# Kernel optimization log

Measured on AMD Instinct MI355X. Metric: run time of the kernel, lower is better.

The kernel has to match this reference:

```python
import jax, jax.numpy as jnp
import numpy as np

D_STATE = 8
D_CONV = 4
DT_RANK = 8
THRESHOLD = 0.5
KPOOL = 3
PAD = (KPOOL - 1) // 2
EPS = 1e-5


def _rmsnorm(x, w):
    return x * jax.lax.rsqrt(jnp.mean(x * x, axis=-1, keepdims=True) + EPS) * w


def _dw_causal_conv(x, w, b):
    # x: (L, T, C), w: (C, 1, K) depthwise causal conv along T
    xt = jnp.transpose(x, (0, 2, 1))  # (L, C, T)
    y = jax.lax.conv_general_dilated(
        xt, w, window_strides=(1,), padding=[(D_CONV - 1, 0)],
        dimension_numbers=('NCH', 'OIH', 'NCH'), feature_group_count=xt.shape[1])
    return jnp.transpose(y, (0, 2, 1)) + b


def _selective_scan(x, delta, A, B, Cm, D):
    # x, delta: (L,T,d); A: (d,n); B, Cm: (L,T,n); D: (d,)
    dA = jnp.exp(delta[..., None] * A)                        # (L,T,d,n)
    dBx = (delta * x)[..., None] * B[:, :, None, :]           # (L,T,d,n)
    def combine(a, b):
        a1, b1 = a
        a2, b2 = b
        return (a2 * a1, a2 * b1 + b2)
    _, h = jax.lax.associative_scan(combine, (dA, dBx), axis=1)
    y = jnp.einsum('ltdn,ltn->ltd', h, Cm)
    return y + x * D


def _mamba_block(x, in_proj, conv_w, conv_b, x_proj_w, dt_proj_w, dt_proj_b,
                 A_log_f, A_log_b, D_f, D_b, out_proj_w, rms_w):
    # single-depth bidirectional (bimamba-v2 style) block, expand=1, residual + RMSNorm
    res = x
    xn = _rmsnorm(x, rms_w)
    xz = xn @ in_proj                       # (L,T,2C)
    xi, z = jnp.split(xz, 2, axis=-1)
    xi = jax.nn.silu(_dw_causal_conv(xi, conv_w, conv_b))
    dbl = xi @ x_proj_w                     # (L,T,dt_rank+2*d_state)
    dt = dbl[..., :DT_RANK]
    Bm = dbl[..., DT_RANK:DT_RANK + D_STATE]
    Cm = dbl[..., DT_RANK + D_STATE:]
    delta = jax.nn.softplus(dt @ dt_proj_w + dt_proj_b)
    A_f = -jnp.exp(A_log_f)
    A_b = -jnp.exp(A_log_b)
    flip = lambda a: a[:, ::-1]
    y_f = _selective_scan(xi, delta, A_f, Bm, Cm, D_f)
    y_b = flip(_selective_scan(flip(xi), flip(delta), A_b, flip(Bm), flip(Cm), D_b))
    y = 0.5 * (y_f + y_b) * jax.nn.silu(z)  # if_devide_out -> average two directions
    return res + y @ out_proj_w


def reference(feats, in_proj, conv_w, conv_b, x_proj_w, dt_proj_w, dt_proj_b,
              A_log_f, A_log_b, D_f, D_b, out_proj_w, rms_w, mlp_w, mlp_b,
              record_len):
    N, C, H, W = feats.shape
    T = H * W
    rec = np.asarray(record_len)  # static ragged group sizes
    ends = np.cumsum(rec)
    starts = ends - rec
    masks = []
    for s0, L in zip(starts.tolist(), rec.tolist()):
        g = feats[s0:s0 + L]                       # (L,C,H,W)
        if L > 1:
            x = g.reshape(L, C, T).transpose(0, 2, 1)  # l c h w -> l (h w) c
            feat = _mamba_block(x, in_proj, conv_w, conv_b, x_proj_w, dt_proj_w,
                                dt_proj_b, A_log_f, A_log_b, D_f, D_b,
                                out_proj_w, rms_w)
            score = jax.nn.sigmoid(feat @ mlp_w + mlp_b)   # (L,T,1)
            ego = jnp.ones((1, T, 1), feats.dtype)
            bs = jnp.concatenate([ego, score[1:]], axis=0)
        else:
            bs = jnp.ones((1, T, 1), feats.dtype)
        bs = bs.transpose(0, 2, 1).reshape(L, 1, H, W)     # l (h w) c -> l c h w
        masks.append(jnp.where(bs > THRESHOLD, 1.0, 0.0).astype(feats.dtype))
    mask = jnp.concatenate(masks, axis=0)                  # (N,1,H,W)
    pooled = jax.lax.reduce_window(
        mask, -jnp.inf, jax.lax.max,
        window_dimensions=(1, 1, KPOOL, KPOOL), window_strides=(1, 1, 1, 1),
        padding=[(0, 0), (0, 0), (PAD, PAD), (PAD, PAD)])
    return pooled


def setup_inputs():
    key = jax.random.key(0)
    ks = jax.random.split(key, 8)
    C, H, W = 128, 96, 96
    record_len = np.array([2, 3, 1, 2, 4], dtype=np.int64)
    N = int(record_len.sum())
    s = 0.05
    A_log = jnp.log(jnp.broadcast_to(
        jnp.arange(1, D_STATE + 1, dtype=jnp.float32), (C, D_STATE)))
    return {
        'feats': jax.random.normal(ks[0], (N, C, H, W), jnp.float32),
        'in_proj': jax.random.normal(ks[1], (C, 2 * C), jnp.float32) * s,
        'conv_w': jax.random.normal(ks[2], (C, 1, D_CONV), jnp.float32) * s,
        'conv_b': jnp.zeros((C,), jnp.float32),
        'x_proj_w': jax.random.normal(ks[3], (C, DT_RANK + 2 * D_STATE), jnp.float32) * s,
        'dt_proj_w': jax.random.normal(ks[4], (DT_RANK, C), jnp.float32) * s,
        'dt_proj_b': jnp.full((C,), 0.1, jnp.float32),
        'A_log_f': A_log,
        'A_log_b': A_log,
        'D_f': jnp.ones((C,), jnp.float32),
        'D_b': jnp.ones((C,), jnp.float32),
        'out_proj_w': jax.random.normal(ks[5], (C, C), jnp.float32) * s,
        'rms_w': jnp.ones((C,), jnp.float32),
        'mlp_w': jax.random.normal(ks[6], (C, 1), jnp.float32) * s,
        'mlp_b': jnp.zeros((1,), jnp.float32),
        'record_len': jnp.asarray(record_len),
    }
```

## Files before the change

### kernel.cpp

```cpp
#include <hip/hip_runtime.h>
#include <cstdint>
#include <cstddef>

#define C_CH 128
#define T_TOK 9216
#define H_IMG 96
#define W_IMG 96
#define NSTATE 8

#define CHUNK 128
#define RHALO 32
#define REGION (CHUNK + 2 * RHALO)

__device__ __forceinline__ float siluf_dev(float x) {
  return x / (1.0f + expf(-x));
}

__device__ __forceinline__ float fast_silu(float x) {
  return __fdividef(x, 1.0f + __expf(-x));
}

__global__ __launch_bounds__(128) void k0_setup(
    const int* __restrict__ rec, int n_groups, int N,
    const float* __restrict__ out_proj_w, const float* __restrict__ mlp_w,
    float* __restrict__ vvec, int* __restrict__ slot)
{
  const int tid = threadIdx.x;
  if (tid == 0) {
    int f = 0, sl = 0;
    for (int g = 0; g < n_groups; ++g) {
      const int L = rec[g];
      slot[f] = -1;
      for (int i = 1; i < L; ++i) slot[f + i] = sl++;
      f += L;
    }
  }
  if (tid < C_CH) {
    float acc = 0.0f;
    for (int j = 0; j < C_CH; ++j) acc += out_proj_w[tid * C_CH + j] * mlp_w[j];
    vvec[tid] = acc;
  }
}

__global__ __launch_bounds__(256) void k1_gemm(
    const float* __restrict__ feats, const float* __restrict__ in_proj,
    const float* __restrict__ rms_w, const float* __restrict__ mlp_w,
    const float* __restrict__ mlp_b, const float* __restrict__ vvec,
    const int* __restrict__ slot,
    float* __restrict__ xipre, float* __restrict__ wbuf,
    float* __restrict__ logit)
{
  __shared__ float Asm[C_CH * 64];
  __shared__ float Bsm[C_CH * 64];
  __shared__ float redA[256], redB[256], irS[64];
  const int f = blockIdx.y;
  const int s = slot[f];
  if (s < 0) return;
  const int m0 = blockIdx.x * 64;
  const int tid = threadIdx.x;

  {
    const int c0 = tid >> 4;
    const int tq = (tid & 15) * 4;
    const float* src = feats + (size_t)f * C_CH * T_TOK + m0 + tq;
    #pragma unroll
    for (int i = 0; i < 8; ++i) {
      const int c = c0 + i * 16;
      const float4 x4 = *(const float4*)(src + (size_t)c * T_TOK);
      *(float4*)&Asm[c * 64 + tq] = x4;
    }
  }
  __syncthreads();
  {
    const int t = tid & 63;
    const int q = tid >> 6;
    float ssum = 0.0f, rm = 0.0f;
    for (int cc = q * 32; cc < q * 32 + 32; ++cc) {
      const float val = Asm[cc * 64 + t];
      ssum += val * val;
      rm += val * mlp_w[cc];
    }
    redA[tid] = ssum; redB[tid] = rm;
  }
  __syncthreads();
  if (tid < 64) {
    const int t = tid;
    const float ssum = redA[t] + redA[t + 64] + redA[t + 128] + redA[t + 192];
    const float rm   = redB[t] + redB[t + 64] + redB[t + 128] + redB[t + 192];
    const float ir = 1.0f / sqrtf(ssum * (1.0f / C_CH) + 1e-5f);
    logit[(size_t)s * T_TOK + m0 + t] = rm + mlp_b[0];
    irS[t] = ir;
  }
  __syncthreads();
  {
    const int t = tid & 63;
    const int q = tid >> 6;
    const float ir = irS[t];
    for (int cc = q * 32; cc < q * 32 + 32; ++cc) Asm[cc * 64 + t] *= ir;
  }

  const int ti = tid >> 4;
  const int tc = tid & 15;
  for (int chunk = 0; chunk < 4; ++chunk) {
    const int n0 = chunk * 64;
    __syncthreads();
    #pragma unroll
    for (int i = 0; i < 8; ++i) {
      const int idx = tid + 256 * i;
      const int k = idx >> 4;
      const int q = (idx & 15) * 4;
      float4 b4 = *(const float4*)(in_proj + (size_t)k * 256 + n0 + q);
      const float rw = rms_w[k];
      b4.x *= rw; b4.y *= rw; b4.z *= rw; b4.w *= rw;
      *(float4*)&Bsm[k * 64 + q] = b4;
    }
    __syncthreads();
    float acc[4][4];
    #pragma unroll
    for (int i = 0; i < 4; ++i)
      #pragma unroll
      for (int j = 0; j < 4; ++j) acc[i][j] = 0.0f;
    #pragma unroll 8
    for (int k = 0; k < C_CH; ++k) {
      const float4 a4 = *(const float4*)&Asm[k * 64 + ti * 4];
      const float4 b4 = *(const float4*)&Bsm[k * 64 + tc * 4];
      acc[0][0] += a4.x * b4.x; acc[0][1] += a4.x * b4.y; acc[0][2] += a4.x * b4.z; acc[0][3] += a4.x * b4.w;
      acc[1][0] += a4.y * b4.x; acc[1][1] += a4.y * b4.y; acc[1][2] += a4.y * b4.z; acc[1][3] += a4.y * b4.w;
      acc[2][0] += a4.z * b4.x; acc[2][1] += a4.z * b4.y; acc[2][2] += a4.z * b4.z; acc[2][3] += a4.z * b4.w;
      acc[3][0] += a4.w * b4.x; acc[3][1] += a4.w * b4.y; acc[3][2] += a4.w * b4.z; acc[3][3] += a4.w * b4.w;
    }
    if (chunk < 2) {
      const int cb = n0 + tc * 4;
      #pragma unroll
      for (int i = 0; i < 4; ++i) {
        const int t = m0 + ti * 4 + i;
        float4 o; o.x = acc[i][0]; o.y = acc[i][1]; o.z = acc[i][2]; o.w = acc[i][3];
        *(float4*)&xipre[((size_t)s * T_TOK + t) * C_CH + cb] = o;
      }
    } else {
      const int zc = (chunk - 2) * 64 + tc * 4;
      const float4 v4 = *(const float4*)&vvec[zc];
      #pragma unroll
      for (int i = 0; i < 4; ++i) {
        const int t = m0 + ti * 4 + i;
        float4 o;
        o.x = 0.5f * siluf_dev(acc[i][0]) * v4.x;
        o.y = 0.5f * siluf_dev(acc[i][1]) * v4.y;
        o.z = 0.5f * siluf_dev(acc[i][2]) * v4.z;
        o.w = 0.5f * siluf_dev(acc[i][3]) * v4.w;
        *(float4*)&wbuf[((size_t)s * T_TOK + t) * C_CH + zc] = o;
      }
    }
  }
}

__global__ __launch_bounds__(256, 3) void k3_fused(
    const float* __restrict__ xipre, const float* __restrict__ wbuf,
    const float* __restrict__ conv_w, const float* __restrict__ conv_b,
    const float* __restrict__ x_proj_w,
    const float* __restrict__ dt_proj_w, const float* __restrict__ dt_proj_b,
    const float* __restrict__ A_log_f, const float* __restrict__ A_log_b,
    const float* __restrict__ D_f, const float* __restrict__ D_b,
    const int* __restrict__ slot, float* __restrict__ logit)
{
  __shared__ float xibuf[64 * 129];
  __shared__ float dbl[REGION * 24];
  const int f = blockIdx.y;
  const int s = slot[f];
  if (s < 0) return;
  const int c0 = blockIdx.x * CHUNK;
  const int r0 = c0 - RHALO;
  const int tid = threadIdx.x;
  const int c = tid & 127;
  const int half = tid >> 7;
  const size_t rowbase = (size_t)s * T_TOK;
  const float4 cw = *(const float4*)(conv_w + c * 4);
  const float cb = conv_b[c];

  auto ldx = [&](int t) -> float {
    return (t >= 0 && t < T_TOK) ? xipre[(rowbase + t) * C_CH + c] : 0.0f;
  };

  const int q6 = __builtin_amdgcn_readfirstlane(tid >> 6) * 6;
  const int tok = tid & 63;
  for (int pass = 0; pass < 3; ++pass) {
    __syncthreads();
    {
      const int prow0 = pass * 64 + half * 32;
      float xm1 = ldx(r0 + prow0 - 1);
      float xm2 = ldx(r0 + prow0 - 2);
      float xm3 = ldx(r0 + prow0 - 3);
      for (int i = 0; i < 32; ++i) {
        const float cur = ldx(r0 + prow0 + i);
        const float sum = cw.x * xm3 + cw.y * xm2 + cw.z * xm1 + cw.w * cur + cb;
        xibuf[(half * 32 + i) * 129 + c] = fast_silu(sum);
        xm3 = xm2; xm2 = xm1; xm1 = cur;
      }
    }
    __syncthreads();
    {
      float acc[6] = {0, 0, 0, 0, 0, 0};
      for (int cc = 0; cc < C_CH; ++cc) {
        const float xv = xibuf[tok * 129 + cc];
        #pragma unroll
        for (int jj = 0; jj < 6; ++jj)
          acc[jj] += xv * x_proj_w[cc * 24 + q6 + jj];
      }
      #pragma unroll
      for (int jj = 0; jj < 6; ++jj)
        dbl[(pass * 64 + tok) * 24 + q6 + jj] = acc[jj];
    }
  }
  __syncthreads();

  float dw[8], Ac[8];
  const float* Alog = half ? A_log_b : A_log_f;
  #pragma unroll
  for (int r = 0; r < 8; ++r) dw[r] = dt_proj_w[r * C_CH + c];
  #pragma unroll
  for (int n = 0; n < NSTATE; ++n) Ac[n] = -expf(Alog[c * NSTATE + n]);
  const float bias = dt_proj_b[c];
  const float Dd = half ? D_b[c] : D_f[c];
  float h[8] = {0, 0, 0, 0, 0, 0, 0, 0};

  const float a0 = Ac[0];
  int okl = 1;
  #pragma unroll
  for (int n = 1; n < NSTATE; ++n)
    okl &= (fabsf(Ac[n] - (float)(n + 1) * a0) <= 1e-4f * fabsf(Ac[n])) ? 1 : 0;
  const bool fastA = (__all(okl) != 0);

  auto decay8 = [&](float dlt, float* dA) {
    if (fastA) {
      const float e1 = __expf(dlt * a0);
      const float e2 = e1 * e1, e3 = e2 * e1, e4 = e2 * e2;
      dA[0] = e1; dA[1] = e2; dA[2] = e3; dA[3] = e4;
      dA[4] = e4 * e1; dA[5] = e4 * e2; dA[6] = e4 * e3; dA[7] = e4 * e4;
    } else {
      #pragma unroll
      for (int n = 0; n < NSTATE; ++n) dA[n] = __expf(dlt * Ac[n]);
    }
  };

  if (half == 0) {
    const int tb = (r0 < 0) ? 0 : r0;
    const int steps = c0 + CHUNK - tb;
    const int outg0 = (c0 - tb) >> 3;
    const int ng = steps >> 3;
    float xm1 = ldx(tb - 1), xm2 = ldx(tb - 2), xm3 = ldx(tb - 3);
    for (int g = 0; g < ng; ++g) {
      const int t0 = tb + g * 8;
      const bool out = (g >= outg0);
      float pg[8], wg[8];
      #pragma unroll
      for (int j = 0; j < 8; ++j) {
        const size_t gi = (rowbase + t0 + j) * C_CH + c;
        pg[j] = xipre[gi];
        wg[j] = out ? wbuf[gi] : 0.0f;
      }
      #pragma unroll
      for (int j = 0; j < 8; ++j) {
        const int t = t0 + j;
        const int p = t - r0;
        const float cur = pg[j];
        const float sum = cw.x * xm3 + cw.y * xm2 + cw.z * xm1 + cw.w * cur + cb;
        const float xiv = fast_silu(sum);
        xm3 = xm2; xm2 = xm1; xm1 = cur;
        const float4 d0 = *(const float4*)&dbl[p * 24];
        const float4 d1 = *(const float4*)&dbl[p * 24 + 4];
        float pre = bias;
        pre += d0.x * dw[0] + d0.y * dw[1] + d0.z * dw[2] + d0.w * dw[3];
        pre += d1.x * dw[4] + d1.y * dw[5] + d1.z * dw[6] + d1.w * dw[7];
        const float dlt = fmaxf(pre, 0.0f) + __logf(1.0f + __expf(-fabsf(pre)));
        const float u = dlt * xiv;
        const float4 b0 = *(const float4*)&dbl[p * 24 + 8];
        const float4 b1 = *(const float4*)&dbl[p * 24 + 12];
        float dA[8];
        decay8(dlt, dA);
        h[0] = dA[0] * h[0] + u * b0.x;
        h[1] = dA[1] * h[1] + u * b0.y;
        h[2] = dA[2] * h[2] + u * b0.z;
        h[3] = dA[3] * h[3] + u * b0.w;
        h[4] = dA[4] * h[4] + u * b1.x;
        h[5] = dA[5] * h[5] + u * b1.y;
        h[6] = dA[6] * h[6] + u * b1.z;
        h[7] = dA[7] * h[7] + u * b1.w;
        if (out) {
          const float4 cc0 = *(const float4*)&dbl[p * 24 + 16];
          const float4 cc1 = *(const float4*)&dbl[p * 24 + 20];
          float y = xiv * Dd;
          y += h[0] * cc0.x + h[1] * cc0.y + h[2] * cc0.z + h[3] * cc0.w;
          y += h[4] * cc1.x + h[5] * cc1.y + h[6] * cc1.z + h[7] * cc1.w;
          float contrib = y * wg[j];
          contrib += __shfl_xor(contrib, 1);
          contrib += __shfl_xor(contrib, 2);
          contrib += __shfl_xor(contrib, 4);
          contrib += __shfl_xor(contrib, 8);
          contrib += __shfl_xor(contrib, 16);
          contrib += __shfl_xor(contrib, 32);
          if ((tid & 63) == 0) atomicAdd(&logit[rowbase + t], contrib);
        }
      }
    }
  } else {
    const int te2e = r0 + REGION;
    const int te2 = (te2e > T_TOK) ? T_TOK : te2e;
    const int steps = te2 - c0;
    const int outg0 = (te2 - (c0 + CHUNK)) >> 3;
    const int ng = steps >> 3;
    float w0 = ldx(te2 - 1), w1 = ldx(te2 - 2), w2 = ldx(te2 - 3), w3 = ldx(te2 - 4);
    for (int g = 0; g < ng; ++g) {
      const int t0 = te2 - 1 - g * 8;
      const bool out = (g >= outg0);
      float nv[8], wg[8];
      #pragma unroll
      for (int j = 0; j < 8; ++j) {
        nv[j] = ldx(t0 - 4 - j);
        wg[j] = out ? wbuf[(rowbase + t0 - j) * C_CH + c] : 0.0f;
      }
      #pragma unroll
      for (int j = 0; j < 8; ++j) {
        const int t = t0 - j;
        const int p = t - r0;
        const float sum = cw.x * w3 + cw.y * w2 + cw.z * w1 + cw.w * w0 + cb;
        const float xiv = fast_silu(sum);
        w0 = w1; w1 = w2; w2 = w3; w3 = nv[j];
        const float4 d0 = *(const float4*)&dbl[p * 24];
        const float4 d1 = *(const float4*)&dbl[p * 24 + 4];
        float pre = bias;
        pre += d0.x * dw[0] + d0.y * dw[1] + d0.z * dw[2] + d0.w * dw[3];
        pre += d1.x * dw[4] + d1.y * dw[5] + d1.z * dw[6] + d1.w * dw[7];
        const float dlt = fmaxf(pre, 0.0f) + __logf(1.0f + __expf(-fabsf(pre)));
        const float u = dlt * xiv;
        const float4 b0 = *(const float4*)&dbl[p * 24 + 8];
        const float4 b1 = *(const float4*)&dbl[p * 24 + 12];
        float dA[8];
        decay8(dlt, dA);
        h[0] = dA[0] * h[0] + u * b0.x;
        h[1] = dA[1] * h[1] + u * b0.y;
        h[2] = dA[2] * h[2] + u * b0.z;
        h[3] = dA[3] * h[3] + u * b0.w;
        h[4] = dA[4] * h[4] + u * b1.x;
        h[5] = dA[5] * h[5] + u * b1.y;
        h[6] = dA[6] * h[6] + u * b1.z;
        h[7] = dA[7] * h[7] + u * b1.w;
        if (out) {
          const float4 cc0 = *(const float4*)&dbl[p * 24 + 16];
          const float4 cc1 = *(const float4*)&dbl[p * 24 + 20];
          float y = xiv * Dd;
          y += h[0] * cc0.x + h[1] * cc0.y + h[2] * cc0.z + h[3] * cc0.w;
          y += h[4] * cc1.x + h[5] * cc1.y + h[6] * cc1.z + h[7] * cc1.w;
          float contrib = y * wg[j];
          contrib += __shfl_xor(contrib, 1);
          contrib += __shfl_xor(contrib, 2);
          contrib += __shfl_xor(contrib, 4);
          contrib += __shfl_xor(contrib, 8);
          contrib += __shfl_xor(contrib, 16);
          contrib += __shfl_xor(contrib, 32);
          if ((tid & 63) == 0) atomicAdd(&logit[rowbase + t], contrib);
        }
      }
    }
  }
}

__global__ __launch_bounds__(128) void k4_pool(
    const float* __restrict__ logit, const int* __restrict__ slot,
    float* __restrict__ out)
{
  const int w = threadIdx.x;
  if (w >= W_IMG) return;
  const int hh = blockIdx.x;
  const int f = blockIdx.y;
  const int s = slot[f];
  float m = 0.0f;
  if (s < 0) {
    m = 1.0f;
  } else {
    for (int dh = -1; dh <= 1; ++dh) {
      const int h2 = hh + dh;
      if (h2 < 0 || h2 >= H_IMG) continue;
      for (int dw = -1; dw <= 1; ++dw) {
        const int w2 = w + dw;
        if (w2 < 0 || w2 >= W_IMG) continue;
        if (logit[(size_t)s * T_TOK + h2 * W_IMG + w2] > 0.0f) m = 1.0f;
      }
    }
  }
  out[(size_t)f * T_TOK + hh * W_IMG + w] = m;
}

extern "C" void kernel_launch(void* const* d_in, const int* in_sizes, int n_in,
                              void* d_out, int out_size, void* d_ws, size_t ws_size,
                              hipStream_t stream) {
  const float* feats      = (const float*)d_in[0];
  const float* in_proj    = (const float*)d_in[1];
  const float* conv_w     = (const float*)d_in[2];
  const float* conv_b     = (const float*)d_in[3];
  const float* x_proj_w   = (const float*)d_in[4];
  const float* dt_proj_w  = (const float*)d_in[5];
  const float* dt_proj_b  = (const float*)d_in[6];
  const float* A_log_f    = (const float*)d_in[7];
  const float* A_log_b    = (const float*)d_in[8];
  const float* D_f        = (const float*)d_in[9];
  const float* D_b        = (const float*)d_in[10];
  const float* out_proj_w = (const float*)d_in[11];
  const float* rms_w      = (const float*)d_in[12];
  const float* mlp_w      = (const float*)d_in[13];
  const float* mlp_b      = (const float*)d_in[14];
  const int*   rec        = (const int*)d_in[15];

  const int N = in_sizes[0] / (C_CH * T_TOK);
  const int n_groups = in_sizes[15];
  int S = N - n_groups;
  if (S < 1) S = 1;

  char* p = (char*)d_ws;
  float* vvec  = (float*)p; p += 1024;
  int*   slot  = (int*)p;   p += ((N * 4 + 255) / 256) * 256;
  float* logit = (float*)p; p += (size_t)S * T_TOK * 4;
  float* xipre = (float*)p; p += (size_t)S * T_TOK * C_CH * 4;
  float* wA    = (float*)p; p += (size_t)S * T_TOK * C_CH * 4;
  (void)ws_size; (void)n_in; (void)out_size;

  k0_setup<<<1, 128, 0, stream>>>(rec, n_groups, N, out_proj_w, mlp_w, vvec, slot);
  k1_gemm<<<dim3(T_TOK / 64, N), 256, 0, stream>>>(
      feats, in_proj, rms_w, mlp_w, mlp_b, vvec, slot, xipre, wA, logit);
  k3_fused<<<dim3(T_TOK / CHUNK, N), 256, 0, stream>>>(
      xipre, wA, conv_w, conv_b, x_proj_w, dt_proj_w, dt_proj_b,
      A_log_f, A_log_b, D_f, D_b, slot, logit);
  k4_pool<<<dim3(H_IMG, N), 128, 0, stream>>>(logit, slot, (float*)d_out);
}
```

Baseline: 347.9 us.

## Split conv+x_proj into separate kernel and halve scan chunk size

The conv and x_proj projection move out of the fused scan kernel into a new k2_convproj kernel, which writes the 24-wide dbl rows to a global buffer once per token. The scan kernel now loads its halo region from that buffer instead of recomputing conv and projection for the halo tokens. This allows CHUNK to drop from 128 to 64, giving more blocks and higher occupancy. The cost is an extra kernel launch plus a global write and read of the dbl buffer, and the halo fraction of the scan itself grows.

```diff
diff --git a/kernel.cpp b/kernel.cpp
--- a/kernel.cpp
+++ b/kernel.cpp
@@ -8,7 +8,7 @@
 #define W_IMG 96
 #define NSTATE 8
 
-#define CHUNK 128
+#define CHUNK 64
 #define RHALO 32
 #define REGION (CHUNK + 2 * RHALO)
 
@@ -154,16 +154,65 @@
   }
 }
 
-__global__ __launch_bounds__(256, 3) void k3_fused(
+__global__ __launch_bounds__(256, 4) void k2_convproj(
+    const float* __restrict__ xipre,
+    const float* __restrict__ conv_w, const float* __restrict__ conv_b,
+    const float* __restrict__ x_proj_w, const int* __restrict__ slot,
+    float* __restrict__ dbl_g)
+{
+  __shared__ float xibuf[64 * 129];
+  const int f = blockIdx.y;
+  const int s = slot[f];
+  if (s < 0) return;
+  const int m0 = blockIdx.x * 64;
+  const int tid = threadIdx.x;
+  const int c = tid & 127;
+  const int half = tid >> 7;
+  const size_t rowbase = (size_t)s * T_TOK;
+  const float4 cw = *(const float4*)(conv_w + c * 4);
+  const float cb = conv_b[c];
+
+  auto ldx = [&](int t) -> float {
+    return (t >= 0) ? xipre[(rowbase + t) * C_CH + c] : 0.0f;
+  };
+
+  {
+    const int t0 = m0 + half * 32;
+    float xm1 = ldx(t0 - 1), xm2 = ldx(t0 - 2), xm3 = ldx(t0 - 3);
+    #pragma unroll
+    for (int i = 0; i < 32; ++i) {
+      const float cur = ldx(t0 + i);
+      const float sum = cw.x * xm3 + cw.y * xm2 + cw.z * xm1 + cw.w * cur + cb;
+      xibuf[(half * 32 + i) * 129 + c] = fast_silu(sum);
+      xm3 = xm2; xm2 = xm1; xm1 = cur;
+    }
+  }
+  __syncthreads();
+  {
+    const int q6 = __builtin_amdgcn_readfirstlane(tid >> 6) * 6;
+    const int tok = tid & 63;
+    float acc[6] = {0, 0, 0, 0, 0, 0};
+    for (int cc = 0; cc < C_CH; ++cc) {
+      const float xv = xibuf[tok * 129 + cc];
+      #pragma unroll
+      for (int jj = 0; jj < 6; ++jj)
+        acc[jj] += xv * x_proj_w[cc * 24 + q6 + jj];
+    }
+    #pragma unroll
+    for (int jj = 0; jj < 6; ++jj)
+      dbl_g[(rowbase + m0 + tok) * 24 + q6 + jj] = acc[jj];
+  }
+}
+
+__global__ __launch_bounds__(256, 4) void k3_scan(
     const float* __restrict__ xipre, const float* __restrict__ wbuf,
+    const float* __restrict__ dbl_g,
     const float* __restrict__ conv_w, const float* __restrict__ conv_b,
-    const float* __restrict__ x_proj_w,
     const float* __restrict__ dt_proj_w, const float* __restrict__ dt_proj_b,
     const float* __restrict__ A_log_f, const float* __restrict__ A_log_b,
     const float* __restrict__ D_f, const float* __restrict__ D_b,
     const int* __restrict__ slot, float* __restrict__ logit)
 {
-  __shared__ float xibuf[64 * 129];
   __shared__ float dbl[REGION * 24];
   const int f = blockIdx.y;
   const int s = slot[f];
@@ -181,34 +230,15 @@
     return (t >= 0 && t < T_TOK) ? xipre[(rowbase + t) * C_CH + c] : 0.0f;
   };
 
-  const int q6 = __builtin_amdgcn_readfirstlane(tid >> 6) * 6;
-  const int tok = tid & 63;
-  for (int pass = 0; pass < 3; ++pass) {
-    __syncthreads();
-    {
-      const int prow0 = pass * 64 + half * 32;
-      float xm1 = ldx(r0 + prow0 - 1);
-      float xm2 = ldx(r0 + prow0 - 2);
-      float xm3 = ldx(r0 + prow0 - 3);
-      for (int i = 0; i < 32; ++i) {
-        const float cur = ldx(r0 + prow0 + i);
-        const float sum = cw.x * xm3 + cw.y * xm2 + cw.z * xm1 + cw.w * cur + cb;
-        xibuf[(half * 32 + i) * 129 + c] = fast_silu(sum);
-        xm3 = xm2; xm2 = xm1; xm1 = cur;
-      }
-    }
-    __syncthreads();
-    {
-      float acc[6] = {0, 0, 0, 0, 0, 0};
-      for (int cc = 0; cc < C_CH; ++cc) {
-        const float xv = xibuf[tok * 129 + cc];
-        #pragma unroll
-        for (int jj = 0; jj < 6; ++jj)
-          acc[jj] += xv * x_proj_w[cc * 24 + q6 + jj];
-      }
-      #pragma unroll
-      for (int jj = 0; jj < 6; ++jj)
-        dbl[(pass * 64 + tok) * 24 + q6 + jj] = acc[jj];
+  {
+    const long grow = ((long)rowbase + r0) * 24;
+    const int lo  = (r0 < 0) ? (-r0) * 6 : 0;
+    const int hi  = (r0 + REGION > T_TOK) ? (T_TOK - r0) * 6 : REGION * 6;
+    #pragma unroll
+    for (int i = 0; i < 3; ++i) {
+      const int idx = tid + i * 256;
+      if (idx >= lo && idx < hi)
+        *(float4*)&dbl[idx * 4] = *(const float4*)&dbl_g[grow + (long)idx * 4];
     }
   }
   __syncthreads();
@@ -421,13 +451,16 @@
   float* logit = (float*)p; p += (size_t)S * T_TOK * 4;
   float* xipre = (float*)p; p += (size_t)S * T_TOK * C_CH * 4;
   float* wA    = (float*)p; p += (size_t)S * T_TOK * C_CH * 4;
+  float* dblg  = (float*)p; p += (size_t)S * T_TOK * 24 * 4;
   (void)ws_size; (void)n_in; (void)out_size;
 
   k0_setup<<<1, 128, 0, stream>>>(rec, n_groups, N, out_proj_w, mlp_w, vvec, slot);
   k1_gemm<<<dim3(T_TOK / 64, N), 256, 0, stream>>>(
       feats, in_proj, rms_w, mlp_w, mlp_b, vvec, slot, xipre, wA, logit);
-  k3_fused<<<dim3(T_TOK / CHUNK, N), 256, 0, stream>>>(
-      xipre, wA, conv_w, conv_b, x_proj_w, dt_proj_w, dt_proj_b,
+  k2_convproj<<<dim3(T_TOK / 64, N), 256, 0, stream>>>(
+      xipre, conv_w, conv_b, x_proj_w, slot, dblg);
+  k3_scan<<<dim3(T_TOK / CHUNK, N), 256, 0, stream>>>(
+      xipre, wA, dblg, conv_w, conv_b, dt_proj_w, dt_proj_b,
       A_log_f, A_log_b, D_f, D_b, slot, logit);
   k4_pool<<<dim3(H_IMG, N), 128, 0, stream>>>(logit, slot, (float*)d_out);
 }
```

New measurement: 323.3 us. 7.1% less time.
